# Kernel optimization log

Hardware: AMD Instinct MI355X
Metric: run time of the kernel (lower is better)

Reference implementation:

```python
import jax, jax.numpy as jnp
import numpy as np

VOCAB, EMB, H, L, B, S = 100000, 300, 256, 2, 64, 512


def _lstm_cell(x, h, c, w_ih, w_hh, b_ih, b_hh):
    # PyTorch gate order: i, f, g, o
    g = x @ w_ih.T + h @ w_hh.T + (b_ih + b_hh)
    i, f, gg, o = jnp.split(g, 4, axis=-1)
    i, f, o = jax.nn.sigmoid(i), jax.nn.sigmoid(f), jax.nn.sigmoid(o)
    c_new = f * c + i * jnp.tanh(gg)
    h_new = o * jnp.tanh(c_new)
    return h_new, c_new


def setup_inputs() -> dict:
    key = jax.random.key(0)
    ks = jax.random.split(key, 16)
    k = 1.0 / np.sqrt(H)
    u = lambda kk, shape: jax.random.uniform(kk, shape, jnp.float32, -k, k)
    inp = {
        "contexts": jax.random.randint(ks[0], (B, S), 0, VOCAB),
        "positions": jax.random.randint(ks[1], (B,), 0, S),
        "emb": jax.random.normal(ks[2], (VOCAB, EMB), jnp.float32) * 0.1,
        # layer 0: input width EMB; layer 1: input width 2H. dim0 = direction (fwd, bwd)
        "w_ih_l0": u(ks[3], (2, 4 * H, EMB)),
        "w_hh_l0": u(ks[4], (2, 4 * H, H)),
        "b_ih_l0": u(ks[5], (2, 4 * H)),
        "b_hh_l0": u(ks[6], (2, 4 * H)),
        "w_ih_l1": u(ks[7], (2, 4 * H, 2 * H)),
        "w_hh_l1": u(ks[8], (2, 4 * H, H)),
        "b_ih_l1": u(ks[9], (2, 4 * H)),
        "b_hh_l1": u(ks[10], (2, 4 * H)),
        "w_cls": u(ks[11], (2, 2 * H)),
        "b_cls": u(ks[12], (2,)),
    }
    return inp


def reference(emb, w_ih_l0, w_hh_l0, b_ih_l0, b_hh_l0,
              w_ih_l1, w_hh_l1, b_ih_l1, b_hh_l1,
              w_cls, b_cls, contexts, positions):
    layers = [(w_ih_l0, w_hh_l0, b_ih_l0, b_hh_l0),
              (w_ih_l1, w_hh_l1, b_ih_l1, b_hh_l1)]
    bsz = contexts.shape[0]

    def step(carry, tok):
        h, c = carry  # (L, 2, B, H) each
        x = emb[tok]  # (B, EMB) — per-timestep embedding gather
        new_h, new_c = [], []
        for l, (wih, whh, bih, bhh) in enumerate(layers):
            outs = []
            # NOTE: original calls the bidirectional LSTM with seq_len=1 while
            # threading hidden state, so BOTH directions step forward in time.
            for d in range(2):
                hh, cc = _lstm_cell(x, h[l, d], c[l, d], wih[d], whh[d], bih[d], bhh[d])
                outs.append(hh); new_h.append(hh); new_c.append(cc)
            x = jnp.concatenate(outs, axis=-1)  # (B, 2H) -> input to next layer
        h = jnp.stack(new_h).reshape(len(layers), 2, bsz, H)
        c = jnp.stack(new_c).reshape(len(layers), 2, bsz, H)
        return (h, c), x

    h0 = jnp.zeros((len(layers), 2, bsz, H), jnp.float32)
    carry0 = (h0, h0)
    tokens = contexts.T  # (S, B): scan over sequence dim
    _, contexts_encoded = jax.lax.scan(step, carry0, tokens)  # (S, B, 2H)

    # gather encoded state at each item's target position
    target_output = contexts_encoded[positions, jnp.arange(bsz)]  # (B, 2H)
    logits = target_output @ w_cls.T + b_cls  # (B, 2)
    probs = jax.nn.sigmoid(logits)
    return (logits, probs, target_output)
```

## Files before the change

kernel.cpp:

```cpp
#include <hip/hip_runtime.h>
#include <hip/hip_cooperative_groups.h>


typedef short v8s __attribute__((ext_vector_type(8)));
typedef float v4f __attribute__((ext_vector_type(4)));
typedef unsigned long long u64;

#define S_LEN 512
#define BATCH 64
#define EMBD  300
#define XPAD  320
#define ROWP0 584
#define ROWP1 776
#define NWG   256

__device__ inline unsigned short f2bf(float x) {
  union { float f; unsigned u; } v; v.f = x;
  unsigned r = v.u + 0x7FFF + ((v.u >> 16) & 1);
  return (unsigned short)(r >> 16);
}
__device__ inline float sigm(float x) { return 1.f / (1.f + __expf(-x)); }
__device__ inline float tanhf_(float x) {
  float e = __expf(-2.f * fabsf(x));
  float r = (1.f - e) / (1.f + e);
  return x >= 0.f ? r : -r;
}

__device__ inline v8s ld_sys16(const unsigned short* p) {
  union { u64 q[2]; v8s s; } u;
  u.q[0] = __hip_atomic_load((const u64*)p,     __ATOMIC_RELAXED, __HIP_MEMORY_SCOPE_SYSTEM);
  u.q[1] = __hip_atomic_load((const u64*)p + 1, __ATOMIC_RELAXED, __HIP_MEMORY_SCOPE_SYSTEM);
  return u.s;
}
__device__ inline float ldf_sys(const float* p) {
  return __hip_atomic_load(p, __ATOMIC_RELAXED, __HIP_MEMORY_SCOPE_SYSTEM);
}
__device__ inline unsigned ldu_sys(const unsigned* p) {
  return __hip_atomic_load(p, __ATOMIC_RELAXED, __HIP_MEMORY_SCOPE_SYSTEM);
}
__device__ inline void st4_sys(unsigned* p, unsigned v) {
  __hip_atomic_store(p, v, __ATOMIC_RELAXED, __HIP_MEMORY_SCOPE_SYSTEM);
}
__device__ inline void stf_sys(float* p, float v) {
  __hip_atomic_store(p, v, __ATOMIC_RELAXED, __HIP_MEMORY_SCOPE_SYSTEM);
}

__device__ inline void wave_poll(const unsigned* pollp, unsigned thr) {
  if (__all((pollp == nullptr) || (thr == 0u)) ) return;
  for (;;) {
    bool ok = (pollp == nullptr) || (thr == 0u) || (ldu_sys(pollp) >= thr);
    if (__all(ok)) break;
    __builtin_amdgcn_s_sleep(1);
  }
}

template<int NKA, int NKB, int P2OFF>
__device__ inline void mfma_dual(const v8s* a, const unsigned short* t0,
                                 const unsigned short* t1, v4f& acc0, v4f& acc1) {
#pragma unroll
  for (int i = 0; i < NKA; ++i) {
    v8s b0 = *(const v8s*)(t0 + i * 32);
    v8s b1 = *(const v8s*)(t1 + i * 32);
    acc0 = __builtin_amdgcn_mfma_f32_16x16x32_bf16(a[i], b0, acc0, 0, 0, 0);
    acc1 = __builtin_amdgcn_mfma_f32_16x16x32_bf16(a[i], b1, acc1, 0, 0, 0);
  }
#pragma unroll
  for (int i = 0; i < NKB; ++i) {
    v8s b0 = *(const v8s*)(t0 + P2OFF + i * 32);
    v8s b1 = *(const v8s*)(t1 + P2OFF + i * 32);
    acc0 = __builtin_amdgcn_mfma_f32_16x16x32_bf16(a[NKA + i], b0, acc0, 0, 0, 0);
    acc1 = __builtin_amdgcn_mfma_f32_16x16x32_bf16(a[NKA + i], b1, acc1, 0, 0, 0);
  }
}

__global__ void __launch_bounds__(128, 1)
ContextAwareModel_9655086481739_kernel(
    const int* __restrict__ contexts, const int* __restrict__ positions,
    const float* __restrict__ emb,
    const float* __restrict__ wih0, const float* __restrict__ whh0,
    const float* __restrict__ bih0, const float* __restrict__ bhh0,
    const float* __restrict__ wih1, const float* __restrict__ whh1,
    const float* __restrict__ bih1, const float* __restrict__ bhh1,
    const float* __restrict__ wcls, const float* __restrict__ bcls,
    float* __restrict__ out, unsigned char* __restrict__ ws)
{
  __shared__ unsigned short smem[32 * ROWP1];

  const int wg   = blockIdx.x;
  const int tid  = threadIdx.x;
  const int layer  = wg >> 7;
  const int d      = (wg >> 6) & 1;
  const int colblk = (wg >> 1) & 31;
  const int mhalf  = wg & 1;
  const int wv   = tid >> 6;
  const int lane = tid & 63;
  const int quad = lane >> 4;
  const int lc   = lane & 15;
  const int hc0  = colblk * 8;
  const int hc   = hc0 + (lc & 7);
  const int m0   = mhalf * 32 + wv * 16;
  const int r_base = m0 + quad * 4;
  const int gid  = layer * 4 + d * 2 + mhalf;

  unsigned short* Xbuf  = (unsigned short*)ws;
  unsigned short* h0buf = (unsigned short*)(ws + 20971520u);
  unsigned short* h1buf = (unsigned short*)(ws + 20971520u + 262144u);
  float*          tgt   = (float*)(ws + 20971520u + 262144u + 131072u);
  unsigned*       flags = (unsigned*)(ws + 20971520u + 262144u + 131072u + 131072u);

  const int ROWP = layer ? ROWP1 : ROWP0;

  {
    for (int i = wg * 128 + tid; i < 196608; i += NWG * 128) h0buf[i] = 0;
    if (wg == 0) { for (int i = tid; i < 2048; i += 128) flags[i] = 0; }
  }
  {
    int gw2 = wg * 2 + wv;
    for (int rl = 0; rl < 64; ++rl) {
      int rr = gw2 * 64 + rl;
      int t = rr >> 6, b = rr & 63;
      int tok = contexts[b * S_LEN + t];
      const float* erow = emb + (long)tok * EMBD;
#pragma unroll
      for (int i = 0; i < 5; ++i) {
        int kk = i * 64 + lane;
        float v = (kk < EMBD) ? erow[kk] : 0.f;
        if (kk < XPAD) Xbuf[rr * XPAD + kk] = f2bf(v);
      }
    }
  }
  {
    const float* wih = layer ? wih1 : wih0;
    const float* whh = layer ? whh1 : whh0;
    const int KI  = layer ? 512 : 300;
    const int KIp = layer ? 512 : 320;
    const int KT  = layer ? 768 : 576;
    int lr = tid >> 2, sub = tid & 3;
    int c = lr & 15, T = lr >> 4;
    int gate = T * 2 + (c >> 3);
    int j = gate * 256 + hc0 + (c & 7);
    const float* wri = wih + (long)(d * 1024 + j) * KI;
    const float* wrh = whh + (long)(d * 1024 + j) * 256;
    for (int kk = sub; kk < ROWP; kk += 4) {
      float v = 0.f;
      if (kk < KI) v = wri[kk];
      else if (kk >= KIp && kk < KT) v = wrh[kk - KIp];
      smem[lr * ROWP + kk] = f2bf(v);
    }
  }
  float bias0, bias1;
  {
    const float* bi = layer ? bih1 : bih0;
    const float* bh = layer ? bhh1 : bhh0;
    int j0 = ((lc >> 3) & 1) * 256 + hc;
    int j1 = (2 + ((lc >> 3) & 1)) * 256 + hc;
    bias0 = bi[d * 1024 + j0] + bh[d * 1024 + j0];
    bias1 = bi[d * 1024 + j1] + bh[d * 1024 + j1];
  }
  int pos[4];
#pragma unroll
  for (int j = 0; j < 4; ++j) pos[j] = positions[r_base + j];
  float cst[4] = {0.f, 0.f, 0.f, 0.f};
  const unsigned short* lds_t0 = smem + lc * ROWP + quad * 8;
  const unsigned short* lds_t1 = smem + (16 + lc) * ROWP + quad * 8;
  const bool hi = (lc & 8) != 0;

  const unsigned* pollp = nullptr;
  int pollcls = -1;
  if (layer == 0) {
    if (wv == 0) {
      if (lane < 32) { pollp = flags + (gid * 32 + lane) * 8;            pollcls = 0; }
      else           { pollp = flags + ((4 + mhalf) * 32 + lane - 32) * 8; pollcls = 1; }
    } else {
      if (lane < 32) { pollp = flags + ((6 + mhalf) * 32 + lane) * 8;     pollcls = 1; }
    }
  } else {
    if (wv == 0) {
      if (lane < 32) { pollp = flags + (gid * 32 + lane) * 8;            pollcls = 0; }
      else           { pollp = flags + ((0 + mhalf) * 32 + lane - 32) * 8; pollcls = 1; }
    } else {
      if (lane < 32) { pollp = flags + ((2 + mhalf) * 32 + lane) * 8;     pollcls = 1; }
    }
  }
  unsigned* myflag = flags + (gid * 32 + colblk) * 8;

  cooperative_groups::grid_group gg = cooperative_groups::this_grid();
  __syncthreads();
  gg.sync();

  if (layer == 0) {
    for (int t = 0; t < S_LEN; ++t) {
      v8s a[18];
      {
        const unsigned short* aP1 = Xbuf + (t * BATCH + m0 + lc) * XPAD + quad * 8;
#pragma unroll
        for (int i = 0; i < 10; ++i) a[i] = *(const v8s*)(aP1 + i * 32);
      }
      {
        unsigned thr = 0;
        if (pollcls == 0) thr = (unsigned)t;
        else if (pollcls == 1) thr = (t >= 4) ? (unsigned)(t - 3) : 0u;
        wave_poll(pollp, thr);
      }
      __syncthreads();
      {
        const unsigned short* aP2 = h0buf + ((t + 3) & 3) * 32768 + (m0 + lc) * 512 + d * 256 + quad * 8;
#pragma unroll
        for (int i = 0; i < 8; ++i) a[10 + i] = ld_sys16(aP2 + i * 32);
      }
      v4f acc0 = {bias0, bias0, bias0, bias0};
      v4f acc1 = {bias1, bias1, bias1, bias1};
      mfma_dual<10, 8, 320>(a, lds_t0, lds_t1, acc0, acc1);
#pragma unroll
      for (int j = 0; j < 4; ++j) {
        float a0 = acc0[j], a1 = acc1[j];
        float o0 = __shfl_xor(a0, 8);
        float o1 = __shfl_xor(a1, 8);
        float iv = hi ? o0 : a0;
        float fv = hi ? a0 : o0;
        float gv = hi ? o1 : a1;
        float ov = hi ? a1 : o1;
        float ii = sigm(iv), ff = sigm(fv), ggt = tanhf_(gv), oo = sigm(ov);
        float cn = ff * cst[j] + ii * ggt;
        cst[j] = cn;
        float hv = oo * tanhf_(cn);
        unsigned hb = f2bf(hv);
        unsigned ob = ((unsigned)__shfl_xor((int)hb, 1)) & 0xFFFFu;
        if (lc < 8 && !(lc & 1)) {
          unsigned word = hb | (ob << 16);
          st4_sys((unsigned*)&h0buf[(t & 3) * 32768 + (r_base + j) * 512 + d * 256 + hc], word);
        }
      }
      asm volatile("s_waitcnt vmcnt(0)" ::: "memory");
      __syncthreads();
      if (tid == 0) st4_sys(myflag, (unsigned)(t + 1));
    }
  } else {
    for (int t = 0; t < S_LEN; ++t) {
      {
        unsigned thr = (pollcls == 0) ? (unsigned)t
                     : (pollcls == 1) ? (unsigned)(t + 1) : 0u;
        wave_poll(pollp, thr);
      }
      __syncthreads();
      v8s a[24];
      {
        const unsigned short* p = h0buf + (t & 3) * 32768 + (m0 + lc) * 512 + quad * 8;
#pragma unroll
        for (int i = 0; i < 16; ++i) a[i] = ld_sys16(p + i * 32);
      }
      {
        const unsigned short* p = h1buf + ((t + 1) & 1) * 32768 + d * 16384 + (m0 + lc) * 256 + quad * 8;
#pragma unroll
        for (int i = 0; i < 8; ++i) a[16 + i] = ld_sys16(p + i * 32);
      }
      v4f acc0 = {bias0, bias0, bias0, bias0};
      v4f acc1 = {bias1, bias1, bias1, bias1};
      mfma_dual<16, 8, 512>(a, lds_t0, lds_t1, acc0, acc1);
#pragma unroll
      for (int j = 0; j < 4; ++j) {
        float a0 = acc0[j], a1 = acc1[j];
        float o0 = __shfl_xor(a0, 8);
        float o1 = __shfl_xor(a1, 8);
        float iv = hi ? o0 : a0;
        float fv = hi ? a0 : o0;
        float gv = hi ? o1 : a1;
        float ov = hi ? a1 : o1;
        float ii = sigm(iv), ff = sigm(fv), ggt = tanhf_(gv), oo = sigm(ov);
        float cn = ff * cst[j] + ii * ggt;
        cst[j] = cn;
        float hv = oo * tanhf_(cn);
        unsigned hb = f2bf(hv);
        unsigned ob = ((unsigned)__shfl_xor((int)hb, 1)) & 0xFFFFu;
        int r = r_base + j;
        if (lc < 8 && !(lc & 1)) {
          unsigned word = hb | (ob << 16);
          st4_sys((unsigned*)&h1buf[(t & 1) * 32768 + d * 16384 + r * 256 + hc], word);
        }
        if (lc < 8 && pos[j] == t) stf_sys(&tgt[r * 512 + d * 256 + hc], hv);
      }
      asm volatile("s_waitcnt vmcnt(0)" ::: "memory");
      __syncthreads();
      if (tid == 0) st4_sys(myflag, (unsigned)(t + 1));
    }
  }

  {
    int g = (wv == 0) ? 4 : 6;
    const unsigned* jp = flags + ((g + (lane >> 5)) * 32 + (lane & 31)) * 8;
    wave_poll(jp, (unsigned)S_LEN);
  }
  __syncthreads();

  {
    for (int i = wg * 128 + tid; i < BATCH * 512; i += NWG * 128) out[256 + i] = ldf_sys(&tgt[i]);
    int gw = wg * 2 + wv;
    if (gw < 128) {
      int b = gw >> 1, cl2 = gw & 1;
      float s = 0.f;
#pragma unroll
      for (int i = 0; i < 8; ++i) {
        int j = i * 64 + lane;
        s += ldf_sys(&tgt[b * 512 + j]) * wcls[cl2 * 512 + j];
      }
      s += __shfl_xor(s, 32); s += __shfl_xor(s, 16); s += __shfl_xor(s, 8);
      s += __shfl_xor(s, 4);  s += __shfl_xor(s, 2);  s += __shfl_xor(s, 1);
      if (lane == 0) {
        float L = s + bcls[cl2];
        out[b * 2 + cl2] = L;
        out[128 + b * 2 + cl2] = sigm(L);
      }
    }
  }
}

extern "C" void kernel_launch(void* const* d_in, const int* in_sizes, int n_in,
                              void* d_out, int out_size, void* d_ws, size_t ws_size,
                              hipStream_t stream) {
  (void)in_sizes; (void)n_in; (void)out_size; (void)ws_size;
  const int*   contexts  = (const int*)d_in[0];
  const int*   positions = (const int*)d_in[1];
  const float* emb   = (const float*)d_in[2];
  const float* wih0  = (const float*)d_in[3];
  const float* whh0  = (const float*)d_in[4];
  const float* bih0  = (const float*)d_in[5];
  const float* bhh0  = (const float*)d_in[6];
  const float* wih1  = (const float*)d_in[7];
  const float* whh1  = (const float*)d_in[8];
  const float* bih1  = (const float*)d_in[9];
  const float* bhh1  = (const float*)d_in[10];
  const float* wcls  = (const float*)d_in[11];
  const float* bcls  = (const float*)d_in[12];
  float* out = (float*)d_out;
  unsigned char* ws = (unsigned char*)d_ws;

  void* args[] = { &contexts, &positions, &emb,
                   &wih0, &whh0, &bih0, &bhh0,
                   &wih1, &whh1, &bih1, &bhh1,
                   &wcls, &bcls, &out, &ws };
  hipLaunchCooperativeKernel((const void*)ContextAwareModel_9655086481739_kernel,
                             dim3(NWG), dim3(128), args, 0, stream);
}
```

Baseline: 3.078 ms.

## Replace per-step flag barriers with timestamp-tagged hidden-state words

Each bf16 hidden-state pair is now stored as a 64-bit word with the step index in the upper half, so consumers spin directly on the data until every tag matches instead of polling separate per-workgroup flags. This removes the s_waitcnt plus __syncthreads plus flag-store handshake at the end of every timestep, and it lets layer 0 issue its input-projection MFMAs before waiting on the recurrent state. The target outputs are written straight into the output buffer, and a per-wave end flag replaces the final join. In exchange, the state traffic doubles in bytes, every wave now polls 32–64 words per step, and correctness depends on the 64-bit stores being atomic.

```diff
diff --git a/kernel.cpp b/kernel.cpp
--- a/kernel.cpp
+++ b/kernel.cpp
@@ -14,6 +14,11 @@
 #define ROWP1 776
 #define NWG   256
 
+#define H0T_OFF   20971520u
+#define H1T_OFF   (H0T_OFF + 524288u)
+#define EFLAG_OFF (H1T_OFF + 262144u)
+#define ZERO_U64  98432
+
 __device__ inline unsigned short f2bf(float x) {
   union { float f; unsigned u; } v; v.f = x;
   unsigned r = v.u + 0x7FFF + ((v.u >> 16) & 1);
@@ -26,51 +31,23 @@
   return x >= 0.f ? r : -r;
 }
 
-__device__ inline v8s ld_sys16(const unsigned short* p) {
-  union { u64 q[2]; v8s s; } u;
-  u.q[0] = __hip_atomic_load((const u64*)p,     __ATOMIC_RELAXED, __HIP_MEMORY_SCOPE_SYSTEM);
-  u.q[1] = __hip_atomic_load((const u64*)p + 1, __ATOMIC_RELAXED, __HIP_MEMORY_SCOPE_SYSTEM);
-  return u.s;
+__device__ inline u64 ld_sys64(const u64* p) {
+  return __hip_atomic_load(p, __ATOMIC_RELAXED, __HIP_MEMORY_SCOPE_SYSTEM);
+}
+__device__ inline void st8_sys(u64* p, u64 v) {
+  __hip_atomic_store(p, v, __ATOMIC_RELAXED, __HIP_MEMORY_SCOPE_SYSTEM);
+}
+__device__ inline unsigned ldu_sys(const unsigned* p) {
+  return __hip_atomic_load(p, __ATOMIC_RELAXED, __HIP_MEMORY_SCOPE_SYSTEM);
+}
+__device__ inline void st4_sys(unsigned* p, unsigned v) {
+  __hip_atomic_store(p, v, __ATOMIC_RELAXED, __HIP_MEMORY_SCOPE_SYSTEM);
+}
+__device__ inline void stf_sys(float* p, float v) {
+  __hip_atomic_store(p, v, __ATOMIC_RELAXED, __HIP_MEMORY_SCOPE_SYSTEM);
 }
 __device__ inline float ldf_sys(const float* p) {
   return __hip_atomic_load(p, __ATOMIC_RELAXED, __HIP_MEMORY_SCOPE_SYSTEM);
-}
-__device__ inline unsigned ldu_sys(const unsigned* p) {
-  return __hip_atomic_load(p, __ATOMIC_RELAXED, __HIP_MEMORY_SCOPE_SYSTEM);
-}
-__device__ inline void st4_sys(unsigned* p, unsigned v) {
-  __hip_atomic_store(p, v, __ATOMIC_RELAXED, __HIP_MEMORY_SCOPE_SYSTEM);
-}
-__device__ inline void stf_sys(float* p, float v) {
-  __hip_atomic_store(p, v, __ATOMIC_RELAXED, __HIP_MEMORY_SCOPE_SYSTEM);
-}
-
-__device__ inline void wave_poll(const unsigned* pollp, unsigned thr) {
-  if (__all((pollp == nullptr) || (thr == 0u)) ) return;
-  for (;;) {
-    bool ok = (pollp == nullptr) || (thr == 0u) || (ldu_sys(pollp) >= thr);
-    if (__all(ok)) break;
-    __builtin_amdgcn_s_sleep(1);
-  }
-}
-
-template<int NKA, int NKB, int P2OFF>
-__device__ inline void mfma_dual(const v8s* a, const unsigned short* t0,
-                                 const unsigned short* t1, v4f& acc0, v4f& acc1) {
-#pragma unroll
-  for (int i = 0; i < NKA; ++i) {
-    v8s b0 = *(const v8s*)(t0 + i * 32);
-    v8s b1 = *(const v8s*)(t1 + i * 32);
-    acc0 = __builtin_amdgcn_mfma_f32_16x16x32_bf16(a[i], b0, acc0, 0, 0, 0);
-    acc1 = __builtin_amdgcn_mfma_f32_16x16x32_bf16(a[i], b1, acc1, 0, 0, 0);
-  }
-#pragma unroll
-  for (int i = 0; i < NKB; ++i) {
-    v8s b0 = *(const v8s*)(t0 + P2OFF + i * 32);
-    v8s b1 = *(const v8s*)(t1 + P2OFF + i * 32);
-    acc0 = __builtin_amdgcn_mfma_f32_16x16x32_bf16(a[NKA + i], b0, acc0, 0, 0, 0);
-    acc1 = __builtin_amdgcn_mfma_f32_16x16x32_bf16(a[NKA + i], b1, acc1, 0, 0, 0);
-  }
 }
 
 __global__ void __launch_bounds__(128, 1)
@@ -100,19 +77,19 @@
   const int hc   = hc0 + (lc & 7);
   const int m0   = mhalf * 32 + wv * 16;
   const int r_base = m0 + quad * 4;
-  const int gid  = layer * 4 + d * 2 + mhalf;
-
-  unsigned short* Xbuf  = (unsigned short*)ws;
-  unsigned short* h0buf = (unsigned short*)(ws + 20971520u);
-  unsigned short* h1buf = (unsigned short*)(ws + 20971520u + 262144u);
-  float*          tgt   = (float*)(ws + 20971520u + 262144u + 131072u);
-  unsigned*       flags = (unsigned*)(ws + 20971520u + 262144u + 131072u + 131072u);
+
+  unsigned short* Xbuf = (unsigned short*)ws;
+  u64*      h0t   = (u64*)(ws + H0T_OFF);
+  u64*      h1t   = (u64*)(ws + H1T_OFF);
+  unsigned* eflag = (unsigned*)(ws + EFLAG_OFF);
+  float*    tgt   = out + 256;
 
   const int ROWP = layer ? ROWP1 : ROWP0;
 
   {
-    for (int i = wg * 128 + tid; i < 196608; i += NWG * 128) h0buf[i] = 0;
-    if (wg == 0) { for (int i = tid; i < 2048; i += 128) flags[i] = 0; }
+    u64* zp = (u64*)(ws + H0T_OFF);
+    for (int i = wg * 128 + tid; i < ZERO_U64; i += NWG * 128)
+      st8_sys(zp + i, 0ull);
   }
   {
     int gw2 = wg * 2 + wv;
@@ -165,52 +142,60 @@
   const unsigned short* lds_t1 = smem + (16 + lc) * ROWP + quad * 8;
   const bool hi = (lc & 8) != 0;
 
-  const unsigned* pollp = nullptr;
-  int pollcls = -1;
-  if (layer == 0) {
-    if (wv == 0) {
-      if (lane < 32) { pollp = flags + (gid * 32 + lane) * 8;            pollcls = 0; }
-      else           { pollp = flags + ((4 + mhalf) * 32 + lane - 32) * 8; pollcls = 1; }
-    } else {
-      if (lane < 32) { pollp = flags + ((6 + mhalf) * 32 + lane) * 8;     pollcls = 1; }
-    }
-  } else {
-    if (wv == 0) {
-      if (lane < 32) { pollp = flags + (gid * 32 + lane) * 8;            pollcls = 0; }
-      else           { pollp = flags + ((0 + mhalf) * 32 + lane - 32) * 8; pollcls = 1; }
-    } else {
-      if (lane < 32) { pollp = flags + ((2 + mhalf) * 32 + lane) * 8;     pollcls = 1; }
-    }
-  }
-  unsigned* myflag = flags + (gid * 32 + colblk) * 8;
-
   cooperative_groups::grid_group gg = cooperative_groups::this_grid();
   __syncthreads();
   gg.sync();
 
   if (layer == 0) {
     for (int t = 0; t < S_LEN; ++t) {
-      v8s a[18];
+      v4f acc0 = {bias0, bias0, bias0, bias0};
+      v4f acc1 = {bias1, bias1, bias1, bias1};
       {
         const unsigned short* aP1 = Xbuf + (t * BATCH + m0 + lc) * XPAD + quad * 8;
 #pragma unroll
-        for (int i = 0; i < 10; ++i) a[i] = *(const v8s*)(aP1 + i * 32);
-      }
-      {
-        unsigned thr = 0;
-        if (pollcls == 0) thr = (unsigned)t;
-        else if (pollcls == 1) thr = (t >= 4) ? (unsigned)(t - 3) : 0u;
-        wave_poll(pollp, thr);
-      }
-      __syncthreads();
-      {
-        const unsigned short* aP2 = h0buf + ((t + 3) & 3) * 32768 + (m0 + lc) * 512 + d * 256 + quad * 8;
-#pragma unroll
-        for (int i = 0; i < 8; ++i) a[10 + i] = ld_sys16(aP2 + i * 32);
-      }
-      v4f acc0 = {bias0, bias0, bias0, bias0};
-      v4f acc1 = {bias1, bias1, bias1, bias1};
-      mfma_dual<10, 8, 320>(a, lds_t0, lds_t1, acc0, acc1);
+        for (int i = 0; i < 10; ++i) {
+          v8s av = *(const v8s*)(aP1 + i * 32);
+          v8s b0 = *(const v8s*)(lds_t0 + i * 32);
+          v8s b1 = *(const v8s*)(lds_t1 + i * 32);
+          acc0 = __builtin_amdgcn_mfma_f32_16x16x32_bf16(av, b0, acc0, 0, 0, 0);
+          acc1 = __builtin_amdgcn_mfma_f32_16x16x32_bf16(av, b1, acc1, 0, 0, 0);
+        }
+      }
+      if (t > 0) {
+        const u64* hp = h0t + (((t + 3) & 3) * 16384 + (m0 + lc) * 256 + d * 128 + quad * 4);
+        const unsigned T = (unsigned)t;
+        const bool dobp = (t >= 4);
+        const u64* bp = h1t + ((t & 1) * 16384 + m0 * 256 + (lane >> 5) * 128 + (lane & 31) * 4);
+        const unsigned bthr = (unsigned)(t - 3);
+        u64 w[32];
+        for (;;) {
+#pragma unroll
+          for (int i = 0; i < 8; ++i)
+#pragma unroll
+            for (int k = 0; k < 4; ++k)
+              w[i * 4 + k] = ld_sys64(hp + i * 16 + k);
+          unsigned diff = 0;
+#pragma unroll
+          for (int i = 0; i < 32; ++i) diff |= (unsigned)(w[i] >> 32) ^ T;
+          bool ok = (diff == 0);
+          if (dobp) ok = ok && ((unsigned)(ld_sys64(bp) >> 32) >= bthr);
+          if (__all(ok)) break;
+          __builtin_amdgcn_s_sleep(1);
+        }
+#pragma unroll
+        for (int i = 0; i < 8; ++i) {
+          union { unsigned u[4]; v8s s; } f;
+          f.u[0] = (unsigned)w[i * 4 + 0];
+          f.u[1] = (unsigned)w[i * 4 + 1];
+          f.u[2] = (unsigned)w[i * 4 + 2];
+          f.u[3] = (unsigned)w[i * 4 + 3];
+          v8s b0 = *(const v8s*)(lds_t0 + 320 + i * 32);
+          v8s b1 = *(const v8s*)(lds_t1 + 320 + i * 32);
+          acc0 = __builtin_amdgcn_mfma_f32_16x16x32_bf16(f.s, b0, acc0, 0, 0, 0);
+          acc1 = __builtin_amdgcn_mfma_f32_16x16x32_bf16(f.s, b1, acc1, 0, 0, 0);
+        }
+      }
+      const u64 tagbits = ((u64)(unsigned)(t + 1)) << 32;
 #pragma unroll
       for (int j = 0; j < 4; ++j) {
         float a0 = acc0[j], a1 = acc1[j];
@@ -228,35 +213,74 @@
         unsigned ob = ((unsigned)__shfl_xor((int)hb, 1)) & 0xFFFFu;
         if (lc < 8 && !(lc & 1)) {
           unsigned word = hb | (ob << 16);
-          st4_sys((unsigned*)&h0buf[(t & 3) * 32768 + (r_base + j) * 512 + d * 256 + hc], word);
-        }
-      }
-      asm volatile("s_waitcnt vmcnt(0)" ::: "memory");
-      __syncthreads();
-      if (tid == 0) st4_sys(myflag, (unsigned)(t + 1));
+          st8_sys(h0t + ((t & 3) * 16384 + (r_base + j) * 256 + d * 128 + colblk * 4 + (lc >> 1)),
+                  (u64)word | tagbits);
+        }
+      }
     }
   } else {
     for (int t = 0; t < S_LEN; ++t) {
-      {
-        unsigned thr = (pollcls == 0) ? (unsigned)t
-                     : (pollcls == 1) ? (unsigned)(t + 1) : 0u;
-        wave_poll(pollp, thr);
-      }
-      __syncthreads();
-      v8s a[24];
-      {
-        const unsigned short* p = h0buf + (t & 3) * 32768 + (m0 + lc) * 512 + quad * 8;
-#pragma unroll
-        for (int i = 0; i < 16; ++i) a[i] = ld_sys16(p + i * 32);
-      }
-      {
-        const unsigned short* p = h1buf + ((t + 1) & 1) * 32768 + d * 16384 + (m0 + lc) * 256 + quad * 8;
-#pragma unroll
-        for (int i = 0; i < 8; ++i) a[16 + i] = ld_sys16(p + i * 32);
-      }
       v4f acc0 = {bias0, bias0, bias0, bias0};
       v4f acc1 = {bias1, bias1, bias1, bias1};
-      mfma_dual<16, 8, 512>(a, lds_t0, lds_t1, acc0, acc1);
+      if (t > 0) {
+        const u64* hp = h1t + ((((t + 1) & 1)) * 16384 + (m0 + lc) * 256 + d * 128 + quad * 4);
+        const unsigned T = (unsigned)t;
+        u64 w[32];
+        for (;;) {
+#pragma unroll
+          for (int i = 0; i < 8; ++i)
+#pragma unroll
+            for (int k = 0; k < 4; ++k)
+              w[i * 4 + k] = ld_sys64(hp + i * 16 + k);
+          unsigned diff = 0;
+#pragma unroll
+          for (int i = 0; i < 32; ++i) diff |= (unsigned)(w[i] >> 32) ^ T;
+          if (__all(diff == 0)) break;
+          __builtin_amdgcn_s_sleep(1);
+        }
+#pragma unroll
+        for (int i = 0; i < 8; ++i) {
+          union { unsigned u[4]; v8s s; } f;
+          f.u[0] = (unsigned)w[i * 4 + 0];
+          f.u[1] = (unsigned)w[i * 4 + 1];
+          f.u[2] = (unsigned)w[i * 4 + 2];
+          f.u[3] = (unsigned)w[i * 4 + 3];
+          v8s b0 = *(const v8s*)(lds_t0 + 512 + i * 32);
+          v8s b1 = *(const v8s*)(lds_t1 + 512 + i * 32);
+          acc0 = __builtin_amdgcn_mfma_f32_16x16x32_bf16(f.s, b0, acc0, 0, 0, 0);
+          acc1 = __builtin_amdgcn_mfma_f32_16x16x32_bf16(f.s, b1, acc1, 0, 0, 0);
+        }
+      }
+      {
+        const u64* hp = h0t + ((t & 3) * 16384 + (m0 + lc) * 256 + quad * 4);
+        const unsigned T = (unsigned)(t + 1);
+        u64 w[64];
+        for (;;) {
+#pragma unroll
+          for (int i = 0; i < 16; ++i)
+#pragma unroll
+            for (int k = 0; k < 4; ++k)
+              w[i * 4 + k] = ld_sys64(hp + i * 16 + k);
+          unsigned diff = 0;
+#pragma unroll
+          for (int i = 0; i < 64; ++i) diff |= (unsigned)(w[i] >> 32) ^ T;
+          if (__all(diff == 0)) break;
+          __builtin_amdgcn_s_sleep(1);
+        }
+#pragma unroll
+        for (int i = 0; i < 16; ++i) {
+          union { unsigned u[4]; v8s s; } f;
+          f.u[0] = (unsigned)w[i * 4 + 0];
+          f.u[1] = (unsigned)w[i * 4 + 1];
+          f.u[2] = (unsigned)w[i * 4 + 2];
+          f.u[3] = (unsigned)w[i * 4 + 3];
+          v8s b0 = *(const v8s*)(lds_t0 + i * 32);
+          v8s b1 = *(const v8s*)(lds_t1 + i * 32);
+          acc0 = __builtin_amdgcn_mfma_f32_16x16x32_bf16(f.s, b0, acc0, 0, 0, 0);
+          acc1 = __builtin_amdgcn_mfma_f32_16x16x32_bf16(f.s, b1, acc1, 0, 0, 0);
+        }
+      }
+      const u64 tagbits = ((u64)(unsigned)(t + 1)) << 32;
 #pragma unroll
       for (int j = 0; j < 4; ++j) {
         float a0 = acc0[j], a1 = acc1[j];
@@ -275,33 +299,32 @@
         int r = r_base + j;
         if (lc < 8 && !(lc & 1)) {
           unsigned word = hb | (ob << 16);
-          st4_sys((unsigned*)&h1buf[(t & 1) * 32768 + d * 16384 + r * 256 + hc], word);
+          st8_sys(h1t + ((t & 1) * 16384 + r * 256 + d * 128 + colblk * 4 + (lc >> 1)),
+                  (u64)word | tagbits);
         }
         if (lc < 8 && pos[j] == t) stf_sys(&tgt[r * 512 + d * 256 + hc], hv);
       }
-      asm volatile("s_waitcnt vmcnt(0)" ::: "memory");
-      __syncthreads();
-      if (tid == 0) st4_sys(myflag, (unsigned)(t + 1));
-    }
-  }
-
-  {
-    int g = (wv == 0) ? 4 : 6;
-    const unsigned* jp = flags + ((g + (lane >> 5)) * 32 + (lane & 31)) * 8;
-    wave_poll(jp, (unsigned)S_LEN);
-  }
-  __syncthreads();
-
-  {
-    for (int i = wg * 128 + tid; i < BATCH * 512; i += NWG * 128) out[256 + i] = ldf_sys(&tgt[i]);
+    }
+    asm volatile("s_waitcnt vmcnt(0)" ::: "memory");
+    st4_sys(eflag + (wg - 128) * 2 + wv, 1u);
+  }
+
+  {
     int gw = wg * 2 + wv;
     if (gw < 128) {
+      for (;;) {
+        bool ok = true;
+#pragma unroll
+        for (int k = 0; k < 4; ++k) ok &= (ldu_sys(eflag + k * 64 + lane) != 0u);
+        if (__all(ok)) break;
+        __builtin_amdgcn_s_sleep(4);
+      }
       int b = gw >> 1, cl2 = gw & 1;
       float s = 0.f;
 #pragma unroll
       for (int i = 0; i < 8; ++i) {
-        int j = i * 64 + lane;
-        s += ldf_sys(&tgt[b * 512 + j]) * wcls[cl2 * 512 + j];
+        int jj = i * 64 + lane;
+        s += ldf_sys(&tgt[b * 512 + jj]) * wcls[cl2 * 512 + jj];
       }
       s += __shfl_xor(s, 32); s += __shfl_xor(s, 16); s += __shfl_xor(s, 8);
       s += __shfl_xor(s, 4);  s += __shfl_xor(s, 2);  s += __shfl_xor(s, 1);
```

Result: slower. 4.972 ms (+61.6%).

## Replace per-workgroup flags with per-wave sentinel slots and early X-projection overlap

Applied to the files above, without the earlier changes.

Synchronization now uses per-wave sentinels indexed by timestep ring slot instead of per-workgroup flags with a workgroup barrier. Each wave publishes its own progress and polls only the sentinels it needs, which removes the __syncthreads before and after each step. In layer 0 the input-projection MFMAs run before polling for the recurrent state, so that compute overlaps the wait. h0 is no longer zeroed because t=0 skips the recurrent term, tgt is written straight into the output, and the final grid-wide wait is reduced to end flags polled only by the classifier waves. Removing the zeroing risks correctness if the ring-slot logic is wrong, and per-wave polling issues more flag loads.

```diff
diff --git a/kernel.cpp b/kernel.cpp
--- a/kernel.cpp
+++ b/kernel.cpp
@@ -14,6 +14,13 @@
 #define ROWP1 776
 #define NWG   256
 
+#define H0_OFF    20971520u
+#define H1_OFF    (H0_OFF + 262144u)
+#define SENT0_OFF (H1_OFF + 131072u)
+#define SENT1_OFF (SENT0_OFF + 4096u)
+#define EFLAG_OFF (SENT1_OFF + 2048u)
+#define ZERO_U32  1792
+
 __device__ inline unsigned short f2bf(float x) {
   union { float f; unsigned u; } v; v.f = x;
   unsigned r = v.u + 0x7FFF + ((v.u >> 16) & 1);
@@ -32,26 +39,17 @@
   u.q[1] = __hip_atomic_load((const u64*)p + 1, __ATOMIC_RELAXED, __HIP_MEMORY_SCOPE_SYSTEM);
   return u.s;
 }
+__device__ inline unsigned ldu_sys(const unsigned* p) {
+  return __hip_atomic_load(p, __ATOMIC_RELAXED, __HIP_MEMORY_SCOPE_SYSTEM);
+}
+__device__ inline void st4_sys(unsigned* p, unsigned v) {
+  __hip_atomic_store(p, v, __ATOMIC_RELAXED, __HIP_MEMORY_SCOPE_SYSTEM);
+}
+__device__ inline void stf_sys(float* p, float v) {
+  __hip_atomic_store(p, v, __ATOMIC_RELAXED, __HIP_MEMORY_SCOPE_SYSTEM);
+}
 __device__ inline float ldf_sys(const float* p) {
   return __hip_atomic_load(p, __ATOMIC_RELAXED, __HIP_MEMORY_SCOPE_SYSTEM);
-}
-__device__ inline unsigned ldu_sys(const unsigned* p) {
-  return __hip_atomic_load(p, __ATOMIC_RELAXED, __HIP_MEMORY_SCOPE_SYSTEM);
-}
-__device__ inline void st4_sys(unsigned* p, unsigned v) {
-  __hip_atomic_store(p, v, __ATOMIC_RELAXED, __HIP_MEMORY_SCOPE_SYSTEM);
-}
-__device__ inline void stf_sys(float* p, float v) {
-  __hip_atomic_store(p, v, __ATOMIC_RELAXED, __HIP_MEMORY_SCOPE_SYSTEM);
-}
-
-__device__ inline void wave_poll(const unsigned* pollp, unsigned thr) {
-  if (__all((pollp == nullptr) || (thr == 0u)) ) return;
-  for (;;) {
-    bool ok = (pollp == nullptr) || (thr == 0u) || (ldu_sys(pollp) >= thr);
-    if (__all(ok)) break;
-    __builtin_amdgcn_s_sleep(1);
-  }
 }
 
 template<int NKA, int NKB, int P2OFF>
@@ -100,19 +98,21 @@
   const int hc   = hc0 + (lc & 7);
   const int m0   = mhalf * 32 + wv * 16;
   const int r_base = m0 + quad * 4;
-  const int gid  = layer * 4 + d * 2 + mhalf;
 
   unsigned short* Xbuf  = (unsigned short*)ws;
-  unsigned short* h0buf = (unsigned short*)(ws + 20971520u);
-  unsigned short* h1buf = (unsigned short*)(ws + 20971520u + 262144u);
-  float*          tgt   = (float*)(ws + 20971520u + 262144u + 131072u);
-  unsigned*       flags = (unsigned*)(ws + 20971520u + 262144u + 131072u + 131072u);
+  unsigned short* h0buf = (unsigned short*)(ws + H0_OFF);
+  unsigned short* h1buf = (unsigned short*)(ws + H1_OFF);
+  unsigned*       sent0 = (unsigned*)(ws + SENT0_OFF);
+  unsigned*       sent1 = (unsigned*)(ws + SENT1_OFF);
+  unsigned*       eflag = (unsigned*)(ws + EFLAG_OFF);
+  float*          tgt   = out + 256;
 
   const int ROWP = layer ? ROWP1 : ROWP0;
-
-  {
-    for (int i = wg * 128 + tid; i < 196608; i += NWG * 128) h0buf[i] = 0;
-    if (wg == 0) { for (int i = tid; i < 2048; i += 128) flags[i] = 0; }
+  const int sgrp = ((mhalf << 1) | wv) << 5;
+
+  {
+    unsigned* zp = (unsigned*)(ws + SENT0_OFF);
+    for (int i = wg * 128 + tid; i < ZERO_U32; i += NWG * 128) st4_sys(zp + i, 0u);
   }
   {
     int gw2 = wg * 2 + wv;
@@ -164,25 +164,8 @@
   const unsigned short* lds_t0 = smem + lc * ROWP + quad * 8;
   const unsigned short* lds_t1 = smem + (16 + lc) * ROWP + quad * 8;
   const bool hi = (lc & 8) != 0;
-
-  const unsigned* pollp = nullptr;
-  int pollcls = -1;
-  if (layer == 0) {
-    if (wv == 0) {
-      if (lane < 32) { pollp = flags + (gid * 32 + lane) * 8;            pollcls = 0; }
-      else           { pollp = flags + ((4 + mhalf) * 32 + lane - 32) * 8; pollcls = 1; }
-    } else {
-      if (lane < 32) { pollp = flags + ((6 + mhalf) * 32 + lane) * 8;     pollcls = 1; }
-    }
-  } else {
-    if (wv == 0) {
-      if (lane < 32) { pollp = flags + (gid * 32 + lane) * 8;            pollcls = 0; }
-      else           { pollp = flags + ((0 + mhalf) * 32 + lane - 32) * 8; pollcls = 1; }
-    } else {
-      if (lane < 32) { pollp = flags + ((2 + mhalf) * 32 + lane) * 8;     pollcls = 1; }
-    }
-  }
-  unsigned* myflag = flags + (gid * 32 + colblk) * 8;
+  unsigned* myflag = (layer == 0)
+      ? sent0 + 0  : sent1;
 
   cooperative_groups::grid_group gg = cooperative_groups::this_grid();
   __syncthreads();
@@ -190,27 +173,53 @@
 
   if (layer == 0) {
     for (int t = 0; t < S_LEN; ++t) {
-      v8s a[18];
+      const bool needD = (t > 0) && (lane < 32);
+      const bool needB = (t >= 4) && (lane >= 32);
+      const unsigned* sDp = sent0 + ((((t + 3) & 3) * 2 + d) * 4 * 32 + sgrp + (lane & 31));
+      const unsigned* sB0 = sent1 + (((t & 1) * 2 + 0) * 4 * 32 + sgrp + (lane & 31));
+      const unsigned* sB1 = sent1 + (((t & 1) * 2 + 1) * 4 * 32 + sgrp + (lane & 31));
+      unsigned vD = needD ? ldu_sys(sDp) : 0u;
+      unsigned v0 = needB ? ldu_sys(sB0) : 0u;
+      unsigned v1 = needB ? ldu_sys(sB1) : 0u;
+
+      v4f acc0 = {bias0, bias0, bias0, bias0};
+      v4f acc1 = {bias1, bias1, bias1, bias1};
       {
         const unsigned short* aP1 = Xbuf + (t * BATCH + m0 + lc) * XPAD + quad * 8;
 #pragma unroll
-        for (int i = 0; i < 10; ++i) a[i] = *(const v8s*)(aP1 + i * 32);
+        for (int i = 0; i < 10; ++i) {
+          v8s av = *(const v8s*)(aP1 + i * 32);
+          v8s b0 = *(const v8s*)(lds_t0 + i * 32);
+          v8s b1 = *(const v8s*)(lds_t1 + i * 32);
+          acc0 = __builtin_amdgcn_mfma_f32_16x16x32_bf16(av, b0, acc0, 0, 0, 0);
+          acc1 = __builtin_amdgcn_mfma_f32_16x16x32_bf16(av, b1, acc1, 0, 0, 0);
+        }
       }
       {
-        unsigned thr = 0;
-        if (pollcls == 0) thr = (unsigned)t;
-        else if (pollcls == 1) thr = (t >= 4) ? (unsigned)(t - 3) : 0u;
-        wave_poll(pollp, thr);
-      }
-      __syncthreads();
-      {
+        const unsigned thrD = (unsigned)t, thrB = (unsigned)(t - 3);
+        for (;;) {
+          bool ok = (!needD || (vD >= thrD))
+                 && (!needB || ((v0 >= thrB) && (v1 >= thrB)));
+          if (__all(ok)) break;
+          __builtin_amdgcn_s_sleep(1);
+          if (needD) vD = ldu_sys(sDp);
+          if (needB) { v0 = ldu_sys(sB0); v1 = ldu_sys(sB1); }
+        }
+        asm volatile("" ::: "memory");
+      }
+      if (t > 0) {
         const unsigned short* aP2 = h0buf + ((t + 3) & 3) * 32768 + (m0 + lc) * 512 + d * 256 + quad * 8;
-#pragma unroll
-        for (int i = 0; i < 8; ++i) a[10 + i] = ld_sys16(aP2 + i * 32);
-      }
-      v4f acc0 = {bias0, bias0, bias0, bias0};
-      v4f acc1 = {bias1, bias1, bias1, bias1};
-      mfma_dual<10, 8, 320>(a, lds_t0, lds_t1, acc0, acc1);
+        v8s a[8];
+#pragma unroll
+        for (int i = 0; i < 8; ++i) a[i] = ld_sys16(aP2 + i * 32);
+#pragma unroll
+        for (int i = 0; i < 8; ++i) {
+          v8s b0 = *(const v8s*)(lds_t0 + 320 + i * 32);
+          v8s b1 = *(const v8s*)(lds_t1 + 320 + i * 32);
+          acc0 = __builtin_amdgcn_mfma_f32_16x16x32_bf16(a[i], b0, acc0, 0, 0, 0);
+          acc1 = __builtin_amdgcn_mfma_f32_16x16x32_bf16(a[i], b1, acc1, 0, 0, 0);
+        }
+      }
 #pragma unroll
       for (int j = 0; j < 4; ++j) {
         float a0 = acc0[j], a1 = acc1[j];
@@ -232,27 +241,35 @@
         }
       }
       asm volatile("s_waitcnt vmcnt(0)" ::: "memory");
-      __syncthreads();
-      if (tid == 0) st4_sys(myflag, (unsigned)(t + 1));
+      if (lane == 0)
+        st4_sys(sent0 + (((t & 3) * 2 + d) * 4 * 32 + sgrp + colblk), (unsigned)(t + 1));
     }
   } else {
     for (int t = 0; t < S_LEN; ++t) {
+      const bool needA = (t > 0) && (lane < 32);
+      const unsigned* sAp = sent1 + ((((t + 1) & 1) * 2 + d) * 4 * 32 + sgrp + (lane & 31));
+      const unsigned* sBp = sent0 + (((t & 3) * 2 + (lane >> 5)) * 4 * 32 + sgrp + (lane & 31));
+      unsigned vA = needA ? ldu_sys(sAp) : 0u;
+      unsigned vB = ldu_sys(sBp);
       {
-        unsigned thr = (pollcls == 0) ? (unsigned)t
-                     : (pollcls == 1) ? (unsigned)(t + 1) : 0u;
-        wave_poll(pollp, thr);
-      }
-      __syncthreads();
+        const unsigned thrA = (unsigned)t, thrB = (unsigned)(t + 1);
+        for (;;) {
+          bool ok = (!needA || (vA >= thrA)) && (vB >= thrB);
+          if (__all(ok)) break;
+          __builtin_amdgcn_s_sleep(1);
+          if (needA) vA = ldu_sys(sAp);
+          vB = ldu_sys(sBp);
+        }
+        asm volatile("" ::: "memory");
+      }
       v8s a[24];
       {
         const unsigned short* p = h0buf + (t & 3) * 32768 + (m0 + lc) * 512 + quad * 8;
 #pragma unroll
         for (int i = 0; i < 16; ++i) a[i] = ld_sys16(p + i * 32);
-      }
-      {
-        const unsigned short* p = h1buf + ((t + 1) & 1) * 32768 + d * 16384 + (m0 + lc) * 256 + quad * 8;
-#pragma unroll
-        for (int i = 0; i < 8; ++i) a[16 + i] = ld_sys16(p + i * 32);
+        const unsigned short* q = h1buf + ((t + 1) & 1) * 32768 + d * 16384 + (m0 + lc) * 256 + quad * 8;
+#pragma unroll
+        for (int i = 0; i < 8; ++i) a[16 + i] = ld_sys16(q + i * 32);
       }
       v4f acc0 = {bias0, bias0, bias0, bias0};
       v4f acc1 = {bias1, bias1, bias1, bias1};
@@ -280,28 +297,29 @@
         if (lc < 8 && pos[j] == t) stf_sys(&tgt[r * 512 + d * 256 + hc], hv);
       }
       asm volatile("s_waitcnt vmcnt(0)" ::: "memory");
-      __syncthreads();
-      if (tid == 0) st4_sys(myflag, (unsigned)(t + 1));
-    }
-  }
-
-  {
-    int g = (wv == 0) ? 4 : 6;
-    const unsigned* jp = flags + ((g + (lane >> 5)) * 32 + (lane & 31)) * 8;
-    wave_poll(jp, (unsigned)S_LEN);
-  }
-  __syncthreads();
-
-  {
-    for (int i = wg * 128 + tid; i < BATCH * 512; i += NWG * 128) out[256 + i] = ldf_sys(&tgt[i]);
+      if (lane == 0)
+        st4_sys(sent1 + (((t & 1) * 2 + d) * 4 * 32 + sgrp + colblk), (unsigned)(t + 1));
+    }
+    st4_sys(eflag + (wg - 128) * 2 + wv, 1u);
+  }
+
+  {
     int gw = wg * 2 + wv;
     if (gw < 128) {
+      for (;;) {
+        bool ok = true;
+#pragma unroll
+        for (int k = 0; k < 4; ++k) ok &= (ldu_sys(eflag + k * 64 + lane) != 0u);
+        if (__all(ok)) break;
+        __builtin_amdgcn_s_sleep(4);
+      }
+      asm volatile("" ::: "memory");
       int b = gw >> 1, cl2 = gw & 1;
       float s = 0.f;
 #pragma unroll
       for (int i = 0; i < 8; ++i) {
-        int j = i * 64 + lane;
-        s += ldf_sys(&tgt[b * 512 + j]) * wcls[cl2 * 512 + j];
+        int jj = i * 64 + lane;
+        s += ldf_sys(&tgt[b * 512 + jj]) * wcls[cl2 * 512 + jj];
       }
       s += __shfl_xor(s, 32); s += __shfl_xor(s, 16); s += __shfl_xor(s, 8);
       s += __shfl_xor(s, 4);  s += __shfl_xor(s, 2);  s += __shfl_xor(s, 1);
@@ -312,6 +330,7 @@
       }
     }
   }
+  (void)myflag;
 }
 
 extern "C" void kernel_launch(void* const* d_in, const int* in_sizes, int n_in,
```

Result: slower. 3.407 ms (+10.7%).
